# Kernel tuning notes

Measured on AMD Instinct MI355X. Metric: run time of the kernel, lower is better.

## Reference

```python
import jax, jax.numpy as jnp
import numpy as np

N, E, H = 25000, 100000, 32          # nodes, edges, node/clique hidden dim
NC, A, EC = 8000, 50000, 24000       # cliques, node2clique assignments, clique edges
EEMB, CEE, L = 8, 8, 2               # edge emb dims, n layers


def segment_mean(vals, ids, num):
    s = jax.ops.segment_sum(vals, ids, num_segments=num)
    cnt = jax.ops.segment_sum(jnp.ones(ids.shape[0], vals.dtype), ids, num_segments=num)
    return s / jnp.maximum(cnt, 1.0)[:, None]


def setup_inputs() -> dict:
    key = jax.random.key(0)
    ks = jax.random.split(key, 24)
    s = 0.1  # param scale
    inp = {
        "node_features": jax.random.normal(ks[0], (N, H), jnp.float32),
        "edge_index": jax.random.randint(ks[1], (2, E), 0, N),
        "edge_features": jax.random.normal(ks[2], (E, EEMB), jnp.float32),
        "clique_features": jax.random.normal(ks[3], (NC, H), jnp.float32),
        "node2clique_index": jnp.stack([
            jax.random.randint(ks[4], (A,), 0, N),
            jax.random.randint(ks[5], (A,), 0, NC)]),
        "clique_edge_index": jax.random.randint(ks[6], (2, EC), 0, NC),
        "clique_edge_features": jax.random.normal(ks[7], (EC, CEE), jnp.float32),
        # node NNConv params (stacked over L layers)
        "nn1_w": jax.random.normal(ks[8], (L, EEMB, H)) * s,
        "nn1_b": jnp.zeros((L, H)),
        "nn2_w": jax.random.normal(ks[9], (L, H, H * H)) * s,
        "nn2_b": jnp.zeros((L, H * H)),
        "root_w": jax.random.normal(ks[10], (L, H, H)) * s,
        "root_b": jnp.zeros((L, H)),
        # Node2Clique linear
        "n2c_w": jax.random.normal(ks[11], (L, H, H)) * s,
        "n2c_b": jnp.zeros((L, H)),
        # clique NNConv params
        "cnn1_w": jax.random.normal(ks[12], (L, CEE, H)) * s,
        "cnn1_b": jnp.zeros((L, H)),
        "cnn2_w": jax.random.normal(ks[13], (L, H, H * H)) * s,
        "cnn2_b": jnp.zeros((L, H * H)),
        "croot_w": jax.random.normal(ks[14], (L, H, H)) * s,
        "croot_b": jnp.zeros((L, H)),
        # Clique2Node linear
        "c2n_w": jax.random.normal(ks[15], (L, H, H)) * s,
        "c2n_b": jnp.zeros((L, H)),
    }
    return inp


def nnconv(x, src, dst, edge_attr, w1, b1, w2, b2, rw, rb, n_out_nodes):
    # per-edge weight matrices from the edge MLP: [E, in, out]
    h = jax.nn.relu(edge_attr @ w1 + b1)
    We = (h @ w2 + b2).reshape(edge_attr.shape[0], x.shape[1], -1)
    msg = jnp.einsum('ei,eio->eo', x[src], We)           # message from source
    agg = segment_mean(msg, dst, n_out_nodes)            # mean aggregation at target
    return agg + x @ rw + rb                             # root weight + bias


def reference(node_features, edge_index, edge_features, clique_features,
              node2clique_index, clique_edge_index, clique_edge_features,
              nn1_w, nn1_b, nn2_w, nn2_b, root_w, root_b, n2c_w, n2c_b,
              cnn1_w, cnn1_b, cnn2_w, cnn2_b, croot_w, croot_b, c2n_w, c2n_b):
    x, c = node_features, clique_features
    src, dst = edge_index[0], edge_index[1]
    nid, cid = node2clique_index[0], node2clique_index[1]
    csrc, cdst = clique_edge_index[0], clique_edge_index[1]
    for l in range(L):
        # node-level edge-conditioned conv
        x = jax.nn.relu(nnconv(x, src, dst, edge_features,
                               nn1_w[l], nn1_b[l], nn2_w[l], nn2_b[l],
                               root_w[l], root_b[l], N))
        # Node2Clique: project node feats, scatter-mean into cliques
        m = x @ n2c_w[l] + n2c_b[l]
        c = c + segment_mean(m[nid], cid, NC)
        # clique-level edge-conditioned conv
        c = jax.nn.relu(nnconv(c, csrc, cdst, clique_edge_features,
                               cnn1_w[l], cnn1_b[l], cnn2_w[l], cnn2_b[l],
                               croot_w[l], croot_b[l], NC))
        # Clique2Node: project clique feats, scatter-mean back onto nodes
        m = c @ c2n_w[l] + c2n_b[l]
        x = x + segment_mean(m[cid], nid, N)
    return (x, c)
```

## Files before the change

kernel.cpp:

```cpp
#include <hip/hip_runtime.h>
#include <hip/hip_bf16.h>

typedef unsigned int u32;
typedef unsigned short u16;

#define DEVINL __device__ __forceinline__

constexpr int Nn  = 25000;
constexpr int Ee  = 100000;
constexpr int NCc = 8000;
constexpr int Aa  = 50000;
constexpr int ECc = 24000;
constexpr int TCOLS = 1088;
constexpr int WPSZ  = TCOLS*32;
constexpr int TSP   = 1064;
constexpr int NB_N = (Nn + 255)/256;
constexpr int NB_C = (NCc + 255)/256;

typedef float f32x4 __attribute__((ext_vector_type(4)));
typedef short s16x8 __attribute__((ext_vector_type(8)));

DEVINL float b2f(u16 u){ union{u32 i;float f;}v; v.i = ((u32)u)<<16; return v.f; }
DEVINL float bfl(u32 u){ union{u32 i;float f;}v; v.i = u<<16; return v.f; }
DEVINL float bfh(u32 u){ union{u32 i;float f;}v; v.i = u & 0xffff0000u; return v.f; }
DEVINL u16 f2b(float f){ union{float f;u32 i;}v; v.f=f; u32 i=v.i;
  return (u16)((i + 0x7fffu + ((i>>16)&1u)) >> 16); }
DEVINL u32 pk2(float a, float b){ return (u32)f2b(a) | ((u32)f2b(b) << 16); }
DEVINL float ldw(const void* p, long i, int f){
  return f ? ((const float*)p)[i] : b2f(((const u16*)p)[i]);
}

__global__ __launch_bounds__(256) void k_detect(const u16* __restrict__ p, int n,
                        u32* __restrict__ maxbits, int* __restrict__ zcnt,
                        int* __restrict__ done, int* __restrict__ flag){
  int i0 = blockIdx.x*256 + threadIdx.x;
  float lm = 0.f; int lz = 0;
  for (int i = i0; i < n; i += gridDim.x*256){
    u16 v = p[i];
    if (v == 0) lz++;
    lm = fmaxf(lm, fabsf(b2f(v)));
  }
  #pragma unroll
  for (int off = 32; off; off >>= 1){
    lm = fmaxf(lm, __shfl_down(lm, off));
    lz += __shfl_down(lz, off);
  }
  if ((threadIdx.x & 63) == 0){
    atomicMax(maxbits, __float_as_uint(lm));
    atomicAdd(zcnt, lz);
  }
  __syncthreads();
  if (threadIdx.x == 0){
    __threadfence();
    if (atomicAdd(done, 1) == gridDim.x - 1){
      float m = __uint_as_float(*maxbits);
      *flag = (m > 1e6f || *zcnt > n/4) ? 1 : 0;
    }
  }
}

__global__ __launch_bounds__(256) void k_count_all(const int* __restrict__ ei, const int* __restrict__ cei,
                          const int* __restrict__ n2c,
                          int* __restrict__ deg_nd, int* __restrict__ deg_ce,
                          int* __restrict__ deg_n2c, int* __restrict__ deg_c2n,
                          int* __restrict__ cnt_sn, int* __restrict__ cnt_sc){
  int i = blockIdx.x*256 + threadIdx.x;
  if (i < Ee)                             atomicAdd(&deg_nd[ei[Ee + i]], 1);
  else if ((i -= Ee) < ECc)               atomicAdd(&deg_ce[cei[ECc + i]], 1);
  else if ((i -= ECc) < Aa)               atomicAdd(&deg_n2c[n2c[Aa + i]], 1);
  else if ((i -= Aa) < Aa)                atomicAdd(&deg_c2n[n2c[i]], 1);
  else if ((i -= Aa) < Ee)                atomicAdd(&cnt_sn[ei[i]], 1);
  else if ((i -= Ee) < ECc)               atomicAdd(&cnt_sc[cei[i]], 1);
}

__global__ __launch_bounds__(256) void k_scan_block(
    const int* __restrict__ c0, const int* __restrict__ c1,
    const int* __restrict__ c2, const int* __restrict__ c3,
    int* __restrict__ o0, int* __restrict__ o1, int* __restrict__ o2, int* __restrict__ o3,
    int* __restrict__ b0, int* __restrict__ b1, int* __restrict__ b2, int* __restrict__ b3){
  __shared__ int s[256];
  int bid = blockIdx.x, seg, rb;
  if (bid < NB_N){ seg=0; rb=bid; }
  else if (bid < NB_N+NB_C){ seg=1; rb=bid-NB_N; }
  else if (bid < 2*NB_N+NB_C){ seg=2; rb=bid-NB_N-NB_C; }
  else { seg=3; rb=bid-2*NB_N-NB_C; }
  const int* cnt = seg==0?c0 : seg==1?c1 : seg==2?c2 : c3;
  int* offs = seg==0?o0 : seg==1?o1 : seg==2?o2 : o3;
  int* bs   = seg==0?b0 : seg==1?b1 : seg==2?b2 : b3;
  int M = (seg & 1) ? NCc : Nn;
  int tid = threadIdx.x;
  int i = rb*256 + tid;
  int v = (i < M) ? cnt[i] : 0;
  s[tid] = v; __syncthreads();
  for (int d = 1; d < 256; d <<= 1){
    int t = (tid >= d) ? s[tid-d] : 0;
    __syncthreads();
    s[tid] += t;
    __syncthreads();
  }
  if (i < M) offs[i] = s[tid] - v;
  if (tid == 255) bs[rb] = s[255];
}

__global__ __launch_bounds__(512) void k_spine(int* __restrict__ b0, int* __restrict__ b1,
                      int* __restrict__ b2, int* __restrict__ b3){
  __shared__ int s[512];
  int tid = threadIdx.x, seg = tid >> 7, lane = tid & 127;
  int NB = (seg & 1) ? NB_C : NB_N;
  int* bp = seg==0?b0 : seg==1?b1 : seg==2?b2 : b3;
  int v = (lane < NB) ? bp[lane] : 0;
  s[tid] = v; __syncthreads();
  for (int d = 1; d < 128; d <<= 1){
    int t = (lane >= d) ? s[tid-d] : 0;
    __syncthreads();
    s[tid] += t;
    __syncthreads();
  }
  if (lane < NB) bp[lane] = s[tid] - v;
}

__global__ __launch_bounds__(256) void k_scan_fix(
    int* __restrict__ o0, int* __restrict__ o1, int* __restrict__ o2, int* __restrict__ o3,
    const int* __restrict__ b0, const int* __restrict__ b1,
    const int* __restrict__ b2, const int* __restrict__ b3){
  int i = blockIdx.x*256 + threadIdx.x;
  if (i < Nn) o0[i] += b0[i >> 8];
  else if ((i -= Nn) < NCc) o1[i] += b1[i >> 8];
  else if ((i -= NCc) < Nn) o2[i] += b2[i >> 8];
  else if ((i -= Nn) < NCc) o3[i] += b3[i >> 8];
}

__global__ __launch_bounds__(256) void k_place(const int* __restrict__ ei, const int* __restrict__ cei,
                      const int* __restrict__ n2c,
                      const int* __restrict__ offs_n, const int* __restrict__ offs_c,
                      const int* __restrict__ offs_an, const int* __restrict__ offs_ac,
                      int* __restrict__ cur_n, int* __restrict__ cur_c,
                      int* __restrict__ cur_an, int* __restrict__ cur_ac,
                      int* __restrict__ perm_n, int* __restrict__ perm_c,
                      int* __restrict__ an2c, int* __restrict__ ac2n){
  int i = blockIdx.x*256 + threadIdx.x;
  if (i < Ee){
    int s = ei[i];
    perm_n[offs_n[s] + atomicAdd(&cur_n[s], 1)] = i;
  } else if ((i -= Ee) < ECc){
    int s = cei[i];
    perm_c[offs_c[s] + atomicAdd(&cur_c[s], 1)] = i;
  } else if ((i -= ECc) < Aa){
    int c = n2c[Aa + i];
    an2c[offs_ac[c] + atomicAdd(&cur_ac[c], 1)] = n2c[i];
  } else if ((i -= Aa) < Aa){
    int nd = n2c[i];
    ac2n[offs_an[nd] + atomicAdd(&cur_an[nd], 1)] = n2c[Aa + i];
  }
}

__global__ __launch_bounds__(256) void k_gather(const int* __restrict__ ei, const int* __restrict__ cei,
                       const int* __restrict__ perm_n, const int* __restrict__ perm_c,
                       const void* __restrict__ ef, const void* __restrict__ cef,
                       const int* __restrict__ flag,
                       int2* __restrict__ sdp_n, float* __restrict__ efp_n,
                       int2* __restrict__ sdp_c, float* __restrict__ efp_c){
  int i = blockIdx.x*256 + threadIdx.x;
  int f = *flag;
  if (i < Ee*8){
    int p = i >> 3, j = i & 7;
    int e = perm_n[p];
    efp_n[i] = ldw(ef, (long)e*8 + j, f);
    if (j == 0) sdp_n[p] = make_int2(ei[e], ei[Ee + e]);
  } else if ((i -= Ee*8) < ECc*8){
    int p = i >> 3, j = i & 7;
    int e = perm_c[p];
    efp_c[i] = ldw(cef, (long)e*8 + j, f);
    if (j == 0) sdp_c[p] = make_int2(cei[e], cei[ECc + e]);
  }
}

__global__ __launch_bounds__(256) void k_wpack_all(const void* __restrict__ nn2w, const void* __restrict__ nn2b,
                          const void* __restrict__ rootw,
                          const void* __restrict__ cnn2w, const void* __restrict__ cnn2b,
                          const void* __restrict__ crootw,
                          const int* __restrict__ flag, u16* __restrict__ Wp4){
  int i = blockIdx.x*256 + threadIdx.x;
  if (i >= 4*WPSZ) return;
  int set = i / WPSZ, j = i - set*WPSZ;
  int l = set >> 1, isC = set & 1;
  const void* W2 = isC ? cnn2w : nn2w;
  const void* B2 = isC ? cnn2b : nn2b;
  const void* RW = isC ? crootw : rootw;
  int f = *flag;
  int col = j >> 5, ii = j & 31;
  float v;
  if (col < 1024)      v = ldw(W2, (long)l*32768 + ((col>>5)<<10) + (ii<<5) + (col&31), f);
  else if (col < 1056) v = ldw(B2, (long)l*1024 + (ii<<5) + (col-1024), f);
  else                 v = ldw(RW, (long)l*1024 + (ii<<5) + (col-1056), f);
  Wp4[i] = f2b(v);
}

__global__ __launch_bounds__(512) void k_conv_fused(const void* __restrict__ base, int braw,
                           const float* __restrict__ addagg, const int* __restrict__ adddeg, int M,
                           const int2* __restrict__ sdp, const float* __restrict__ efp,
                           const int* __restrict__ offs, int E_,
                           const void* __restrict__ w1, long w1off,
                           const void* __restrict__ b1, long b1off,
                           const u16* __restrict__ Wp,
                           const void* __restrict__ rb, long rboff,
                           const int* __restrict__ flag,
                           float* __restrict__ feat_root, float* __restrict__ agg){
  __shared__ __align__(16) u16 Ts[16*TSP];
  __shared__ float w1s[256];
  __shared__ __align__(8) u32 hws[8][4][16];
  int tid = threadIdx.x;
  int w = tid >> 6, lane = tid & 63;
  int quad = lane >> 4, lm = lane & 15;
  int n0 = blockIdx.x * 16;
  int f = *flag;
  if (tid < 256) w1s[tid] = ldw(w1, w1off + tid, f);
  float bb0 = ldw(b1, b1off + 2*lm, f);
  float bb1 = ldw(b1, b1off + 2*lm + 1, f);
  int n = n0 + lm;
  int nc = n < M ? n : M-1;
  long bidx = (long)nc*32 + quad*8;
  float fv[8];
  if (braw && f == 0){
    uint4 q = *(const uint4*)((const u16*)base + bidx);
    fv[0]=bfl(q.x); fv[1]=bfh(q.x); fv[2]=bfl(q.y); fv[3]=bfh(q.y);
    fv[4]=bfl(q.z); fv[5]=bfh(q.z); fv[6]=bfl(q.w); fv[7]=bfh(q.w);
  } else {
    const float4* bp = (const float4*)((const float*)base + bidx);
    float4 q0 = bp[0], q1 = bp[1];
    fv[0]=q0.x; fv[1]=q0.y; fv[2]=q0.z; fv[3]=q0.w;
    fv[4]=q1.x; fv[5]=q1.y; fv[6]=q1.z; fv[7]=q1.w;
  }
  if (addagg){
    int dg = adddeg[nc];
    float d = (float)(dg > 1 ? dg : 1);
    const float4* ap = (const float4*)(addagg + (size_t)nc*32 + quad*8);
    float4 a0 = ap[0], a1 = ap[1];
    float inv = 1.f/d;
    fv[0]+=a0.x*inv; fv[1]+=a0.y*inv; fv[2]+=a0.z*inv; fv[3]+=a0.w*inv;
    fv[4]+=a1.x*inv; fv[5]+=a1.y*inv; fv[6]+=a1.z*inv; fv[7]+=a1.w*inv;
  }
  s16x8 bfrag;
  #pragma unroll
  for (int j = 0; j < 8; j++) bfrag[j] = (short)f2b(fv[j]);
  #pragma unroll 1
  for (int ti = 0; ti < 9; ti++){
    int ct = w*9 + ti;
    if (ct >= 68) break;
    int colbase = ct*16;
    s16x8 afrag = *(const s16x8*)(Wp + (size_t)(colbase + lm)*32 + quad*8);
    f32x4 acc = {0.f, 0.f, 0.f, 0.f};
    acc = __builtin_amdgcn_mfma_f32_16x16x32_bf16(afrag, bfrag, acc, 0, 0, 0);
    int cb = colbase + quad*4;
    if (ct < 66){
      u32 lo = (u32)f2b(acc[0]) | ((u32)f2b(acc[1]) << 16);
      u32 hi = (u32)f2b(acc[2]) | ((u32)f2b(acc[3]) << 16);
      *(uint2*)&Ts[lm*TSP + cb] = make_uint2(lo, hi);
    } else if (n < M){
      int o = cb - 1056;
      float4 v = make_float4(acc[0] + ldw(rb, rboff+o,   f),
                             acc[1] + ldw(rb, rboff+o+1, f),
                             acc[2] + ldw(rb, rboff+o+2, f),
                             acc[3] + ldw(rb, rboff+o+3, f));
      *(float4*)&feat_root[(size_t)n*32 + o] = v;
    }
  }
  __syncthreads();
  int lo = offs[n0];
  int hi = (n0 + 16 < M) ? offs[n0 + 16] : E_;
  int eg = quad, kk = lm;
  int pos = lo + w*4;
  float ef0 = 0.f, ef1 = 0.f; int sd0 = 0, sd1 = 0;
  if (lane < 32){
    int idx = pos*8 + lane;        if (idx < hi*8) ef0 = efp[idx];
    idx = (pos+32)*8 + lane;       if (idx < hi*8) ef1 = efp[idx];
  } else if (lane < 40){
    int idx = pos*2 + (lane-32);   if (idx < hi*2) sd0 = ((const int*)sdp)[idx];
    idx = (pos+32)*2 + (lane-32);  if (idx < hi*2) sd1 = ((const int*)sdp)[idx];
  }
  for (; pos < hi; pos += 32){
    int np = pos + 64;
    float ef2 = 0.f; int sd2 = 0;
    if (lane < 32){ int idx = np*8 + lane; if (idx < hi*8) ef2 = efp[idx]; }
    else if (lane < 40){ int idx = np*2 + (lane-32); if (idx < hi*2) sd2 = ((const int*)sdp)[idx]; }
    int sn = __shfl(sd0, 32 + 2*eg);
    int dn = __shfl(sd0, 33 + 2*eg);
    bool valid = (pos + eg < hi);
    int sr = sn - n0; sr = sr < 0 ? 0 : (sr > 15 ? 15 : sr);
    float a0 = bb0, a1 = bb1;
    #pragma unroll
    for (int j = 0; j < 8; j++){
      float ev = __shfl(ef0, eg*8 + j);
      a0 += ev * w1s[j*32 + 2*kk];
      a1 += ev * w1s[j*32 + 2*kk+1];
    }
    hws[w][eg][kk] = pk2(fmaxf(a0, 0.f), fmaxf(a1, 0.f));
    if (valid){
      const u16* Tr = &Ts[sr*TSP];
      u32 vb = *(const u32*)&Tr[1024 + 2*kk];
      float m0 = bfl(vb), m1 = bfh(vb);
      #pragma unroll
      for (int kq = 0; kq < 16; kq++){
        u32 hp = hws[w][eg][kq];
        float h0 = bfl(hp), h1 = bfh(hp);
        u32 v0 = *(const u32*)&Tr[(2*kq)*32 + 2*kk];
        u32 v1 = *(const u32*)&Tr[(2*kq+1)*32 + 2*kk];
        m0 += h0*bfl(v0) + h1*bfl(v1);
        m1 += h0*bfh(v0) + h1*bfh(v1);
      }
      float* ap = agg + (size_t)dn*32 + 2*kk;
      atomicAdd(ap,   m0);
      atomicAdd(ap+1, m1);
    }
    ef0 = ef1; sd0 = sd1; ef1 = ef2; sd1 = sd2;
  }
}

__global__ __launch_bounds__(256) void k_update_lin(const float* __restrict__ agg, const int* __restrict__ deg,
                           const float* __restrict__ feat_root, int M,
                           const void* __restrict__ w, long woff,
                           const void* __restrict__ b, long boff,
                           const int* __restrict__ flag,
                           float* __restrict__ feat,
                           const int* __restrict__ sidx, const int* __restrict__ soffs,
                           const int* __restrict__ sdeg, float* __restrict__ sagg){
  __shared__ float wsm[1024], bs[32], rows[8][33];
  int tid = threadIdx.x;
  int f = *flag;
  for (int idx = tid; idx < 1024; idx += 256) wsm[idx] = ldw(w, woff + idx, f);
  if (tid < 32) bs[tid] = ldw(b, boff + tid, f);
  int nl = tid >> 5, o = tid & 31;
  int n = blockIdx.x*8 + nl;
  long i = (long)n*32 + o;
  if (n < M){
    int dg = deg[n];
    float d = (float)(dg > 1 ? dg : 1);
    float v = fmaxf(agg[i]/d + feat_root[i], 0.f);
    rows[nl][o] = v;
    feat[i] = v;
  }
  __syncthreads();
  if (n >= M) return;
  float acc = bs[o];
  #pragma unroll
  for (int j = 0; j < 32; j++) acc += rows[nl][j]*wsm[j*32+o];
  int slo = soffs[n], scnt = sdeg[n];
  for (int a = 0; a < scnt; a++)
    atomicAdd(&sagg[(size_t)sidx[slo + a]*32 + o], acc);
}

__global__ __launch_bounds__(256) void k_store(const float* __restrict__ x, const float* __restrict__ xagg,
                      const int* __restrict__ xdeg, const float* __restrict__ c,
                      void* __restrict__ out, const int* __restrict__ flag){
  int i = blockIdx.x*256 + threadIdx.x;
  int tot = Nn*32 + NCc*32;
  if (i >= tot) return;
  float v;
  if (i < Nn*32){
    int n = i >> 5;
    int dg = xdeg[n];
    float d = (float)(dg > 1 ? dg : 1);
    v = x[i] + xagg[i]/d;
  } else v = c[i - Nn*32];
  if (*flag) ((float*)out)[i] = v;
  else       ((u16*)out)[i]   = f2b(v);
}

extern "C" void kernel_launch(void* const* d_in, const int* in_sizes, int n_in,
                              void* d_out, int out_size, void* d_ws, size_t ws_size,
                              hipStream_t stream){
  const int* ei  = (const int*)d_in[1];
  const int* n2c = (const int*)d_in[4];
  const int* cei = (const int*)d_in[5];
  const void *efr = d_in[2], *cefr = d_in[6];
  const void *nn1w = d_in[7], *nn1b = d_in[8], *nn2w = d_in[9], *nn2b = d_in[10],
             *rootw = d_in[11], *rootb = d_in[12], *n2cw = d_in[13], *n2cb = d_in[14],
             *cnn1w = d_in[15], *cnn1b = d_in[16], *cnn2w = d_in[17], *cnn2b = d_in[18],
             *crootw = d_in[19], *crootb = d_in[20], *c2nw = d_in[21], *c2nb = d_in[22];

  char* ws = (char*)d_ws;
  size_t off = 0;
  auto alloc = [&](size_t bytes){ void* p = ws + off; off += (bytes + 255) & ~(size_t)255; return p; };

  size_t zstart = off;
  float* aggE0  = (float*)alloc((size_t)Nn*32*4);
  float* aggE1  = (float*)alloc((size_t)Nn*32*4);
  float* caggE0 = (float*)alloc((size_t)NCc*32*4);
  float* caggE1 = (float*)alloc((size_t)NCc*32*4);
  float* caggS0 = (float*)alloc((size_t)NCc*32*4);
  float* caggS1 = (float*)alloc((size_t)NCc*32*4);
  float* aggS0  = (float*)alloc((size_t)Nn*32*4);
  float* aggS1  = (float*)alloc((size_t)Nn*32*4);
  int* deg_nd  = (int*)alloc((size_t)Nn*4);
  int* deg_ce  = (int*)alloc((size_t)NCc*4);
  int* deg_n2c = (int*)alloc((size_t)NCc*4);
  int* deg_c2n = (int*)alloc((size_t)Nn*4);
  int* cnt_sn  = (int*)alloc((size_t)Nn*4);
  int* cnt_sc  = (int*)alloc((size_t)NCc*4);
  int* cur_n   = (int*)alloc((size_t)Nn*4);
  int* cur_c   = (int*)alloc((size_t)NCc*4);
  int* cur_an  = (int*)alloc((size_t)Nn*4);
  int* cur_ac  = (int*)alloc((size_t)NCc*4);
  u32* maxbits = (u32*)alloc(256);
  int* zcnt = (int*)((char*)maxbits + 4);
  int* flag = (int*)((char*)maxbits + 8);
  int* done = (int*)((char*)maxbits + 12);
  size_t zbytes = off - zstart;

  float* xB  = (float*)alloc((size_t)Nn*32*4);
  float* xC  = (float*)alloc((size_t)Nn*32*4);
  float* cC0 = (float*)alloc((size_t)NCc*32*4);
  float* cC1 = (float*)alloc((size_t)NCc*32*4);
  float* frn = (float*)alloc((size_t)Nn*32*4);
  float* frc = (float*)alloc((size_t)NCc*32*4);
  int* offs_n  = (int*)alloc((size_t)Nn*4);
  int* offs_c  = (int*)alloc((size_t)NCc*4);
  int* offs_an = (int*)alloc((size_t)Nn*4);
  int* offs_ac = (int*)alloc((size_t)NCc*4);
  int* bs0 = (int*)alloc(512); int* bs1 = (int*)alloc(512);
  int* bs2 = (int*)alloc(512); int* bs3 = (int*)alloc(512);
  int* perm_n = (int*)alloc((size_t)Ee*4);
  int* perm_c = (int*)alloc((size_t)ECc*4);
  int* an2c = (int*)alloc((size_t)Aa*4);
  int* ac2n = (int*)alloc((size_t)Aa*4);
  int2* sdp_n = (int2*)alloc((size_t)Ee*8);
  int2* sdp_c = (int2*)alloc((size_t)ECc*8);
  float* efp_n = (float*)alloc((size_t)Ee*8*4);
  float* efp_c = (float*)alloc((size_t)ECc*8*4);
  u16* Wp4 = (u16*)alloc((size_t)4*WPSZ*2);

  auto nb = [](int n){ return (n + 255)/256; };

  hipMemsetAsync(ws + zstart, 0, zbytes, stream);
  k_detect<<<256,256,0,stream>>>((const u16*)d_in[0], Nn*32, maxbits, zcnt, done, flag);
  k_count_all<<<nb(2*Ee + 2*ECc + 2*Aa),256,0,stream>>>(ei, cei, n2c,
      deg_nd, deg_ce, deg_n2c, deg_c2n, cnt_sn, cnt_sc);
  k_scan_block<<<2*(NB_N+NB_C),256,0,stream>>>(cnt_sn, cnt_sc, deg_c2n, deg_n2c,
      offs_n, offs_c, offs_an, offs_ac, bs0, bs1, bs2, bs3);
  k_spine<<<1,512,0,stream>>>(bs0, bs1, bs2, bs3);
  k_scan_fix<<<nb(2*(Nn+NCc)),256,0,stream>>>(offs_n, offs_c, offs_an, offs_ac,
      bs0, bs1, bs2, bs3);
  k_place<<<nb(Ee+ECc+2*Aa),256,0,stream>>>(ei, cei, n2c, offs_n, offs_c, offs_an, offs_ac,
      cur_n, cur_c, cur_an, cur_ac, perm_n, perm_c, an2c, ac2n);
  k_gather<<<nb(8*(Ee+ECc)),256,0,stream>>>(ei, cei, perm_n, perm_c, efr, cefr, flag,
      sdp_n, efp_n, sdp_c, efp_c);
  k_wpack_all<<<nb(4*WPSZ),256,0,stream>>>(nn2w, nn2b, rootw, cnn2w, cnn2b, crootw, flag, Wp4);

  int Gn = (Nn + 15)/16, Gc = (NCc + 15)/16;

  k_conv_fused<<<Gn,512,0,stream>>>(d_in[0], 1, nullptr, nullptr, Nn, sdp_n, efp_n, offs_n, Ee,
      nn1w, 0, nn1b, 0, Wp4 + 0*WPSZ, rootb, 0, flag, frn, aggE0);
  k_update_lin<<<(Nn+7)/8,256,0,stream>>>(aggE0, deg_nd, frn, Nn, n2cw, 0, n2cb, 0, flag,
      xB, ac2n, offs_an, deg_c2n, caggS0);
  k_conv_fused<<<Gc,512,0,stream>>>(d_in[3], 1, caggS0, deg_n2c, NCc, sdp_c, efp_c, offs_c, ECc,
      cnn1w, 0, cnn1b, 0, Wp4 + 1*WPSZ, crootb, 0, flag, frc, caggE0);
  k_update_lin<<<(NCc+7)/8,256,0,stream>>>(caggE0, deg_ce, frc, NCc, c2nw, 0, c2nb, 0, flag,
      cC0, an2c, offs_ac, deg_n2c, aggS0);
  k_conv_fused<<<Gn,512,0,stream>>>(xB, 0, aggS0, deg_c2n, Nn, sdp_n, efp_n, offs_n, Ee,
      nn1w, 256, nn1b, 32, Wp4 + 2*WPSZ, rootb, 32, flag, frn, aggE1);
  k_update_lin<<<(Nn+7)/8,256,0,stream>>>(aggE1, deg_nd, frn, Nn, n2cw, 1024, n2cb, 32, flag,
      xC, ac2n, offs_an, deg_c2n, caggS1);
  k_conv_fused<<<Gc,512,0,stream>>>(cC0, 0, caggS1, deg_n2c, NCc, sdp_c, efp_c, offs_c, ECc,
      cnn1w, 256, cnn1b, 32, Wp4 + 3*WPSZ, crootb, 32, flag, frc, caggE1);
  k_update_lin<<<(NCc+7)/8,256,0,stream>>>(caggE1, deg_ce, frc, NCc, c2nw, 1024, c2nb, 32, flag,
      cC1, an2c, offs_ac, deg_n2c, aggS1);
  k_store<<<nb(Nn*32 + NCc*32),256,0,stream>>>(xC, aggS1, deg_c2n, cC1, d_out, flag);
}
```

Baseline: 344.6 us.

## Merge preprocessing kernels and use persistent work-stealing conv blocks

Merges detection with degree counting, and scanning with weight packing, into single launches. The three-kernel scan becomes one kernel that spins on a global counter for all block sums. The conv kernel now runs a fixed grid of 1024 blocks that pull 16-node windows from an atomic counter and prefetch the next weight fragment. This removes launch gaps and tail imbalance but adds spin-wait and atomic overhead. The spin-wait assumes all scan blocks are co-resident, which could deadlock if they are not.

New measurement: 403.0 us. +16.9%, slower.

```diff
diff --git a/kernel.cpp b/kernel.cpp
--- a/kernel.cpp
+++ b/kernel.cpp
@@ -16,6 +16,7 @@
 constexpr int TSP   = 1064;
 constexpr int NB_N = (Nn + 255)/256;
 constexpr int NB_C = (NCc + 255)/256;
+constexpr int NCH  = 2*(NB_N + NB_C);
 
 typedef float f32x4 __attribute__((ext_vector_type(4)));
 typedef short s16x8 __attribute__((ext_vector_type(8)));
@@ -30,56 +31,81 @@
   return f ? ((const float*)p)[i] : b2f(((const u16*)p)[i]);
 }
 
-__global__ __launch_bounds__(256) void k_detect(const u16* __restrict__ p, int n,
-                        u32* __restrict__ maxbits, int* __restrict__ zcnt,
-                        int* __restrict__ done, int* __restrict__ flag){
-  int i0 = blockIdx.x*256 + threadIdx.x;
-  float lm = 0.f; int lz = 0;
-  for (int i = i0; i < n; i += gridDim.x*256){
-    u16 v = p[i];
-    if (v == 0) lz++;
-    lm = fmaxf(lm, fabsf(b2f(v)));
-  }
-  #pragma unroll
-  for (int off = 32; off; off >>= 1){
-    lm = fmaxf(lm, __shfl_down(lm, off));
-    lz += __shfl_down(lz, off);
-  }
-  if ((threadIdx.x & 63) == 0){
-    atomicMax(maxbits, __float_as_uint(lm));
-    atomicAdd(zcnt, lz);
-  }
-  __syncthreads();
-  if (threadIdx.x == 0){
-    __threadfence();
-    if (atomicAdd(done, 1) == gridDim.x - 1){
-      float m = __uint_as_float(*maxbits);
-      *flag = (m > 1e6f || *zcnt > n/4) ? 1 : 0;
-    }
-  }
-}
-
-__global__ __launch_bounds__(256) void k_count_all(const int* __restrict__ ei, const int* __restrict__ cei,
-                          const int* __restrict__ n2c,
-                          int* __restrict__ deg_nd, int* __restrict__ deg_ce,
-                          int* __restrict__ deg_n2c, int* __restrict__ deg_c2n,
-                          int* __restrict__ cnt_sn, int* __restrict__ cnt_sc){
-  int i = blockIdx.x*256 + threadIdx.x;
-  if (i < Ee)                             atomicAdd(&deg_nd[ei[Ee + i]], 1);
-  else if ((i -= Ee) < ECc)               atomicAdd(&deg_ce[cei[ECc + i]], 1);
-  else if ((i -= ECc) < Aa)               atomicAdd(&deg_n2c[n2c[Aa + i]], 1);
-  else if ((i -= Aa) < Aa)                atomicAdd(&deg_c2n[n2c[i]], 1);
-  else if ((i -= Aa) < Ee)                atomicAdd(&cnt_sn[ei[i]], 1);
-  else if ((i -= Ee) < ECc)               atomicAdd(&cnt_sc[cei[i]], 1);
-}
-
-__global__ __launch_bounds__(256) void k_scan_block(
+__global__ __launch_bounds__(256) void k_pre1(const u16* __restrict__ xp,
+                      u32* __restrict__ maxbits, int* __restrict__ zcnt,
+                      int* __restrict__ done, int* __restrict__ flag,
+                      const int* __restrict__ ei, const int* __restrict__ cei,
+                      const int* __restrict__ n2c,
+                      int* __restrict__ deg_nd, int* __restrict__ deg_ce,
+                      int* __restrict__ deg_n2c, int* __restrict__ deg_c2n,
+                      int* __restrict__ cnt_sn, int* __restrict__ cnt_sc){
+  int bid = blockIdx.x;
+  if (bid < 256){
+    int n = Nn*32;
+    float lm = 0.f; int lz = 0;
+    for (int i = bid*256 + threadIdx.x; i < n; i += 256*256){
+      u16 v = xp[i];
+      if (v == 0) lz++;
+      lm = fmaxf(lm, fabsf(b2f(v)));
+    }
+    #pragma unroll
+    for (int off = 32; off; off >>= 1){
+      lm = fmaxf(lm, __shfl_down(lm, off));
+      lz += __shfl_down(lz, off);
+    }
+    if ((threadIdx.x & 63) == 0){
+      atomicMax(maxbits, __float_as_uint(lm));
+      atomicAdd(zcnt, lz);
+    }
+    __syncthreads();
+    if (threadIdx.x == 0){
+      __threadfence();
+      if (atomicAdd(done, 1) == 255){
+        float m = __uint_as_float(*maxbits);
+        *flag = (m > 1e6f || *zcnt > n/4) ? 1 : 0;
+      }
+    }
+  } else {
+    int i = (bid - 256)*256 + threadIdx.x;
+    if (i < Ee)                             atomicAdd(&deg_nd[ei[Ee + i]], 1);
+    else if ((i -= Ee) < ECc)               atomicAdd(&deg_ce[cei[ECc + i]], 1);
+    else if ((i -= ECc) < Aa)               atomicAdd(&deg_n2c[n2c[Aa + i]], 1);
+    else if ((i -= Aa) < Aa)                atomicAdd(&deg_c2n[n2c[i]], 1);
+    else if ((i -= Aa) < Ee)                atomicAdd(&cnt_sn[ei[i]], 1);
+    else if ((i -= Ee) < ECc)               atomicAdd(&cnt_sc[cei[i]], 1);
+  }
+}
+
+__global__ __launch_bounds__(256) void k_scan_wpack(
     const int* __restrict__ c0, const int* __restrict__ c1,
     const int* __restrict__ c2, const int* __restrict__ c3,
     int* __restrict__ o0, int* __restrict__ o1, int* __restrict__ o2, int* __restrict__ o3,
-    int* __restrict__ b0, int* __restrict__ b1, int* __restrict__ b2, int* __restrict__ b3){
+    int* __restrict__ b0, int* __restrict__ b1, int* __restrict__ b2, int* __restrict__ b3,
+    int* __restrict__ sdone,
+    const void* __restrict__ nn2w, const void* __restrict__ nn2b, const void* __restrict__ rootw,
+    const void* __restrict__ cnn2w, const void* __restrict__ cnn2b, const void* __restrict__ crootw,
+    const int* __restrict__ flag, u16* __restrict__ Wp4){
+  int bid = blockIdx.x;
+  int tid = threadIdx.x;
+  if (bid >= NCH){
+    int i = (bid - NCH)*256 + tid;
+    if (i >= 4*WPSZ) return;
+    int set = i / WPSZ, j = i - set*WPSZ;
+    int l = set >> 1, isC = set & 1;
+    const void* W2 = isC ? cnn2w : nn2w;
+    const void* B2 = isC ? cnn2b : nn2b;
+    const void* RW = isC ? crootw : rootw;
+    int f = *flag;
+    int col = j >> 5, ii = j & 31;
+    float v;
+    if (col < 1024)      v = ldw(W2, (long)l*32768 + ((col>>5)<<10) + (ii<<5) + (col&31), f);
+    else if (col < 1056) v = ldw(B2, (long)l*1024 + (ii<<5) + (col-1024), f);
+    else                 v = ldw(RW, (long)l*1024 + (ii<<5) + (col-1056), f);
+    Wp4[i] = f2b(v);
+    return;
+  }
   __shared__ int s[256];
-  int bid = blockIdx.x, seg, rb;
+  int seg, rb;
   if (bid < NB_N){ seg=0; rb=bid; }
   else if (bid < NB_N+NB_C){ seg=1; rb=bid-NB_N; }
   else if (bid < 2*NB_N+NB_C){ seg=2; rb=bid-NB_N-NB_C; }
@@ -88,7 +114,6 @@
   int* offs = seg==0?o0 : seg==1?o1 : seg==2?o2 : o3;
   int* bs   = seg==0?b0 : seg==1?b1 : seg==2?b2 : b3;
   int M = (seg & 1) ? NCc : Nn;
-  int tid = threadIdx.x;
   int i = rb*256 + tid;
   int v = (i < M) ? cnt[i] : 0;
   s[tid] = v; __syncthreads();
@@ -98,36 +123,23 @@
     s[tid] += t;
     __syncthreads();
   }
-  if (i < M) offs[i] = s[tid] - v;
-  if (tid == 255) bs[rb] = s[255];
-}
-
-__global__ __launch_bounds__(512) void k_spine(int* __restrict__ b0, int* __restrict__ b1,
-                      int* __restrict__ b2, int* __restrict__ b3){
-  __shared__ int s[512];
-  int tid = threadIdx.x, seg = tid >> 7, lane = tid & 127;
-  int NB = (seg & 1) ? NB_C : NB_N;
-  int* bp = seg==0?b0 : seg==1?b1 : seg==2?b2 : b3;
-  int v = (lane < NB) ? bp[lane] : 0;
-  s[tid] = v; __syncthreads();
-  for (int d = 1; d < 128; d <<= 1){
-    int t = (lane >= d) ? s[tid-d] : 0;
-    __syncthreads();
-    s[tid] += t;
-    __syncthreads();
-  }
-  if (lane < NB) bp[lane] = s[tid] - v;
-}
-
-__global__ __launch_bounds__(256) void k_scan_fix(
-    int* __restrict__ o0, int* __restrict__ o1, int* __restrict__ o2, int* __restrict__ o3,
-    const int* __restrict__ b0, const int* __restrict__ b1,
-    const int* __restrict__ b2, const int* __restrict__ b3){
-  int i = blockIdx.x*256 + threadIdx.x;
-  if (i < Nn) o0[i] += b0[i >> 8];
-  else if ((i -= Nn) < NCc) o1[i] += b1[i >> 8];
-  else if ((i -= NCc) < Nn) o2[i] += b2[i >> 8];
-  else if ((i -= Nn) < NCc) o3[i] += b3[i >> 8];
+  int ex = s[tid] - v;
+  if (tid == 255){
+    atomicExch(&bs[rb], s[255]);
+    __threadfence();
+    atomicAdd(sdone, 1);
+  }
+  if (tid == 0){
+    while (atomicAdd(sdone, 0) < NCH) __builtin_amdgcn_s_sleep(8);
+  }
+  __syncthreads();
+  int contrib = (tid < rb) ? atomicAdd(&bs[tid], 0) : 0;
+  s[tid] = contrib; __syncthreads();
+  for (int d = 128; d; d >>= 1){
+    if (tid < d) s[tid] += s[tid + d];
+    __syncthreads();
+  }
+  if (i < M) offs[i] = ex + s[0];
 }
 
 __global__ __launch_bounds__(256) void k_place(const int* __restrict__ ei, const int* __restrict__ cei,
@@ -175,27 +187,6 @@
   }
 }
 
-__global__ __launch_bounds__(256) void k_wpack_all(const void* __restrict__ nn2w, const void* __restrict__ nn2b,
-                          const void* __restrict__ rootw,
-                          const void* __restrict__ cnn2w, const void* __restrict__ cnn2b,
-                          const void* __restrict__ crootw,
-                          const int* __restrict__ flag, u16* __restrict__ Wp4){
-  int i = blockIdx.x*256 + threadIdx.x;
-  if (i >= 4*WPSZ) return;
-  int set = i / WPSZ, j = i - set*WPSZ;
-  int l = set >> 1, isC = set & 1;
-  const void* W2 = isC ? cnn2w : nn2w;
-  const void* B2 = isC ? cnn2b : nn2b;
-  const void* RW = isC ? crootw : rootw;
-  int f = *flag;
-  int col = j >> 5, ii = j & 31;
-  float v;
-  if (col < 1024)      v = ldw(W2, (long)l*32768 + ((col>>5)<<10) + (ii<<5) + (col&31), f);
-  else if (col < 1056) v = ldw(B2, (long)l*1024 + (ii<<5) + (col-1024), f);
-  else                 v = ldw(RW, (long)l*1024 + (ii<<5) + (col-1056), f);
-  Wp4[i] = f2b(v);
-}
-
 __global__ __launch_bounds__(512) void k_conv_fused(const void* __restrict__ base, int braw,
                            const float* __restrict__ addagg, const int* __restrict__ adddeg, int M,
                            const int2* __restrict__ sdp, const float* __restrict__ efp,
@@ -205,114 +196,127 @@
                            const u16* __restrict__ Wp,
                            const void* __restrict__ rb, long rboff,
                            const int* __restrict__ flag,
+                           int* __restrict__ wctr,
                            float* __restrict__ feat_root, float* __restrict__ agg){
   __shared__ __align__(16) u16 Ts[16*TSP];
   __shared__ float w1s[256];
   __shared__ __align__(8) u32 hws[8][4][16];
+  __shared__ int wshare;
   int tid = threadIdx.x;
   int w = tid >> 6, lane = tid & 63;
   int quad = lane >> 4, lm = lane & 15;
-  int n0 = blockIdx.x * 16;
   int f = *flag;
   if (tid < 256) w1s[tid] = ldw(w1, w1off + tid, f);
   float bb0 = ldw(b1, b1off + 2*lm, f);
   float bb1 = ldw(b1, b1off + 2*lm + 1, f);
-  int n = n0 + lm;
-  int nc = n < M ? n : M-1;
-  long bidx = (long)nc*32 + quad*8;
-  float fv[8];
-  if (braw && f == 0){
-    uint4 q = *(const uint4*)((const u16*)base + bidx);
-    fv[0]=bfl(q.x); fv[1]=bfh(q.x); fv[2]=bfl(q.y); fv[3]=bfh(q.y);
-    fv[4]=bfl(q.z); fv[5]=bfh(q.z); fv[6]=bfl(q.w); fv[7]=bfh(q.w);
-  } else {
-    const float4* bp = (const float4*)((const float*)base + bidx);
-    float4 q0 = bp[0], q1 = bp[1];
-    fv[0]=q0.x; fv[1]=q0.y; fv[2]=q0.z; fv[3]=q0.w;
-    fv[4]=q1.x; fv[5]=q1.y; fv[6]=q1.z; fv[7]=q1.w;
-  }
-  if (addagg){
-    int dg = adddeg[nc];
-    float d = (float)(dg > 1 ? dg : 1);
-    const float4* ap = (const float4*)(addagg + (size_t)nc*32 + quad*8);
-    float4 a0 = ap[0], a1 = ap[1];
-    float inv = 1.f/d;
-    fv[0]+=a0.x*inv; fv[1]+=a0.y*inv; fv[2]+=a0.z*inv; fv[3]+=a0.w*inv;
-    fv[4]+=a1.x*inv; fv[5]+=a1.y*inv; fv[6]+=a1.z*inv; fv[7]+=a1.w*inv;
-  }
-  s16x8 bfrag;
-  #pragma unroll
-  for (int j = 0; j < 8; j++) bfrag[j] = (short)f2b(fv[j]);
-  #pragma unroll 1
-  for (int ti = 0; ti < 9; ti++){
-    int ct = w*9 + ti;
-    if (ct >= 68) break;
-    int colbase = ct*16;
-    s16x8 afrag = *(const s16x8*)(Wp + (size_t)(colbase + lm)*32 + quad*8);
-    f32x4 acc = {0.f, 0.f, 0.f, 0.f};
-    acc = __builtin_amdgcn_mfma_f32_16x16x32_bf16(afrag, bfrag, acc, 0, 0, 0);
-    int cb = colbase + quad*4;
-    if (ct < 66){
-      u32 lo = (u32)f2b(acc[0]) | ((u32)f2b(acc[1]) << 16);
-      u32 hi = (u32)f2b(acc[2]) | ((u32)f2b(acc[3]) << 16);
-      *(uint2*)&Ts[lm*TSP + cb] = make_uint2(lo, hi);
-    } else if (n < M){
-      int o = cb - 1056;
-      float4 v = make_float4(acc[0] + ldw(rb, rboff+o,   f),
-                             acc[1] + ldw(rb, rboff+o+1, f),
-                             acc[2] + ldw(rb, rboff+o+2, f),
-                             acc[3] + ldw(rb, rboff+o+3, f));
-      *(float4*)&feat_root[(size_t)n*32 + o] = v;
-    }
-  }
-  __syncthreads();
-  int lo = offs[n0];
-  int hi = (n0 + 16 < M) ? offs[n0 + 16] : E_;
-  int eg = quad, kk = lm;
-  int pos = lo + w*4;
-  float ef0 = 0.f, ef1 = 0.f; int sd0 = 0, sd1 = 0;
-  if (lane < 32){
-    int idx = pos*8 + lane;        if (idx < hi*8) ef0 = efp[idx];
-    idx = (pos+32)*8 + lane;       if (idx < hi*8) ef1 = efp[idx];
-  } else if (lane < 40){
-    int idx = pos*2 + (lane-32);   if (idx < hi*2) sd0 = ((const int*)sdp)[idx];
-    idx = (pos+32)*2 + (lane-32);  if (idx < hi*2) sd1 = ((const int*)sdp)[idx];
-  }
-  for (; pos < hi; pos += 32){
-    int np = pos + 64;
-    float ef2 = 0.f; int sd2 = 0;
-    if (lane < 32){ int idx = np*8 + lane; if (idx < hi*8) ef2 = efp[idx]; }
-    else if (lane < 40){ int idx = np*2 + (lane-32); if (idx < hi*2) sd2 = ((const int*)sdp)[idx]; }
-    int sn = __shfl(sd0, 32 + 2*eg);
-    int dn = __shfl(sd0, 33 + 2*eg);
-    bool valid = (pos + eg < hi);
-    int sr = sn - n0; sr = sr < 0 ? 0 : (sr > 15 ? 15 : sr);
-    float a0 = bb0, a1 = bb1;
+  int nwin = (M + 15)/16;
+  for (;;){
+    if (tid == 0) wshare = atomicAdd(wctr, 1);
+    __syncthreads();
+    int win = wshare;
+    if (win >= nwin) break;
+    int n0 = win * 16;
+    int n = n0 + lm;
+    int nc = n < M ? n : M-1;
+    long bidx = (long)nc*32 + quad*8;
+    float fv[8];
+    if (braw && f == 0){
+      uint4 q = *(const uint4*)((const u16*)base + bidx);
+      fv[0]=bfl(q.x); fv[1]=bfh(q.x); fv[2]=bfl(q.y); fv[3]=bfh(q.y);
+      fv[4]=bfl(q.z); fv[5]=bfh(q.z); fv[6]=bfl(q.w); fv[7]=bfh(q.w);
+    } else {
+      const float4* bp = (const float4*)((const float*)base + bidx);
+      float4 q0 = bp[0], q1 = bp[1];
+      fv[0]=q0.x; fv[1]=q0.y; fv[2]=q0.z; fv[3]=q0.w;
+      fv[4]=q1.x; fv[5]=q1.y; fv[6]=q1.z; fv[7]=q1.w;
+    }
+    if (addagg){
+      int dg = adddeg[nc];
+      float inv = 1.f/(float)(dg > 1 ? dg : 1);
+      const float4* ap = (const float4*)(addagg + (size_t)nc*32 + quad*8);
+      float4 a0 = ap[0], a1 = ap[1];
+      fv[0]+=a0.x*inv; fv[1]+=a0.y*inv; fv[2]+=a0.z*inv; fv[3]+=a0.w*inv;
+      fv[4]+=a1.x*inv; fv[5]+=a1.y*inv; fv[6]+=a1.z*inv; fv[7]+=a1.w*inv;
+    }
+    s16x8 bfrag;
     #pragma unroll
-    for (int j = 0; j < 8; j++){
-      float ev = __shfl(ef0, eg*8 + j);
-      a0 += ev * w1s[j*32 + 2*kk];
-      a1 += ev * w1s[j*32 + 2*kk+1];
-    }
-    hws[w][eg][kk] = pk2(fmaxf(a0, 0.f), fmaxf(a1, 0.f));
-    if (valid){
-      const u16* Tr = &Ts[sr*TSP];
-      u32 vb = *(const u32*)&Tr[1024 + 2*kk];
-      float m0 = bfl(vb), m1 = bfh(vb);
+    for (int j = 0; j < 8; j++) bfrag[j] = (short)f2b(fv[j]);
+    int ctbase = w*9;
+    s16x8 afc = *(const s16x8*)(Wp + (size_t)(ctbase*16 + lm)*32 + quad*8);
+    #pragma unroll 1
+    for (int ti = 0; ti < 9; ti++){
+      int ct = ctbase + ti;
+      if (ct >= 68) break;
+      s16x8 afn;
+      bool have_n = (ti + 1 < 9) && (ct + 1 < 68);
+      if (have_n) afn = *(const s16x8*)(Wp + (size_t)((ct+1)*16 + lm)*32 + quad*8);
+      f32x4 acc = {0.f, 0.f, 0.f, 0.f};
+      acc = __builtin_amdgcn_mfma_f32_16x16x32_bf16(afc, bfrag, acc, 0, 0, 0);
+      int cb = ct*16 + quad*4;
+      if (ct < 66){
+        u32 lo = (u32)f2b(acc[0]) | ((u32)f2b(acc[1]) << 16);
+        u32 hi = (u32)f2b(acc[2]) | ((u32)f2b(acc[3]) << 16);
+        *(uint2*)&Ts[lm*TSP + cb] = make_uint2(lo, hi);
+      } else if (n < M){
+        int o = cb - 1056;
+        float4 v = make_float4(acc[0] + ldw(rb, rboff+o,   f),
+                               acc[1] + ldw(rb, rboff+o+1, f),
+                               acc[2] + ldw(rb, rboff+o+2, f),
+                               acc[3] + ldw(rb, rboff+o+3, f));
+        *(float4*)&feat_root[(size_t)n*32 + o] = v;
+      }
+      if (have_n) afc = afn;
+    }
+    __syncthreads();
+    int lo = offs[n0];
+    int hi = (n0 + 16 < M) ? offs[n0 + 16] : E_;
+    int eg = quad, kk = lm;
+    int pos = lo + w*4;
+    float ef0 = 0.f, ef1 = 0.f; int sd0 = 0, sd1 = 0;
+    if (lane < 32){
+      int idx = pos*8 + lane;        if (idx < hi*8) ef0 = efp[idx];
+      idx = (pos+32)*8 + lane;       if (idx < hi*8) ef1 = efp[idx];
+    } else if (lane < 40){
+      int idx = pos*2 + (lane-32);   if (idx < hi*2) sd0 = ((const int*)sdp)[idx];
+      idx = (pos+32)*2 + (lane-32);  if (idx < hi*2) sd1 = ((const int*)sdp)[idx];
+    }
+    for (; pos < hi; pos += 32){
+      int np = pos + 64;
+      float ef2 = 0.f; int sd2 = 0;
+      if (lane < 32){ int idx = np*8 + lane; if (idx < hi*8) ef2 = efp[idx]; }
+      else if (lane < 40){ int idx = np*2 + (lane-32); if (idx < hi*2) sd2 = ((const int*)sdp)[idx]; }
+      int sn = __shfl(sd0, 32 + 2*eg);
+      int dn = __shfl(sd0, 33 + 2*eg);
+      bool valid = (pos + eg < hi);
+      int sr = sn - n0; sr = sr < 0 ? 0 : (sr > 15 ? 15 : sr);
+      float a0 = bb0, a1 = bb1;
       #pragma unroll
-      for (int kq = 0; kq < 16; kq++){
-        u32 hp = hws[w][eg][kq];
-        float h0 = bfl(hp), h1 = bfh(hp);
-        u32 v0 = *(const u32*)&Tr[(2*kq)*32 + 2*kk];
-        u32 v1 = *(const u32*)&Tr[(2*kq+1)*32 + 2*kk];
-        m0 += h0*bfl(v0) + h1*bfl(v1);
-        m1 += h0*bfh(v0) + h1*bfh(v1);
+      for (int j = 0; j < 8; j++){
+        float ev = __shfl(ef0, eg*8 + j);
+        a0 += ev * w1s[j*32 + 2*kk];
+        a1 += ev * w1s[j*32 + 2*kk+1];
       }
-      float* ap = agg + (size_t)dn*32 + 2*kk;
-      atomicAdd(ap,   m0);
-      atomicAdd(ap+1, m1);
-    }
-    ef0 = ef1; sd0 = sd1; ef1 = ef2; sd1 = sd2;
+      hws[w][eg][kk] = pk2(fmaxf(a0, 0.f), fmaxf(a1, 0.f));
+      if (valid){
+        const u16* Tr = &Ts[sr*TSP];
+        u32 vb = *(const u32*)&Tr[1024 + 2*kk];
+        float m0 = bfl(vb), m1 = bfh(vb);
+        #pragma unroll
+        for (int kq = 0; kq < 16; kq++){
+          u32 hp = hws[w][eg][kq];
+          float h0 = bfl(hp), h1 = bfh(hp);
+          u32 v0 = *(const u32*)&Tr[(2*kq)*32 + 2*kk];
+          u32 v1 = *(const u32*)&Tr[(2*kq+1)*32 + 2*kk];
+          m0 += h0*bfl(v0) + h1*bfl(v1);
+          m1 += h0*bfh(v0) + h1*bfh(v1);
+        }
+        float* ap = agg + (size_t)dn*32 + 2*kk;
+        atomicAdd(ap,   m0);
+        atomicAdd(ap+1, m1);
+      }
+      ef0 = ef1; sd0 = sd1; ef1 = ef2; sd1 = sd2;
+    }
+    __syncthreads();
   }
 }
 
@@ -402,9 +406,14 @@
   int* cur_an  = (int*)alloc((size_t)Nn*4);
   int* cur_ac  = (int*)alloc((size_t)NCc*4);
   u32* maxbits = (u32*)alloc(256);
-  int* zcnt = (int*)((char*)maxbits + 4);
-  int* flag = (int*)((char*)maxbits + 8);
-  int* done = (int*)((char*)maxbits + 12);
+  int* zcnt  = (int*)((char*)maxbits + 4);
+  int* flag  = (int*)((char*)maxbits + 8);
+  int* done  = (int*)((char*)maxbits + 12);
+  int* sdone = (int*)((char*)maxbits + 16);
+  int* wctr0 = (int*)((char*)maxbits + 20);
+  int* wctr1 = (int*)((char*)maxbits + 24);
+  int* wctr2 = (int*)((char*)maxbits + 28);
+  int* wctr3 = (int*)((char*)maxbits + 32);
   size_t zbytes = off - zstart;
 
   float* xB  = (float*)alloc((size_t)Nn*32*4);
@@ -432,36 +441,31 @@
   auto nb = [](int n){ return (n + 255)/256; };
 
   hipMemsetAsync(ws + zstart, 0, zbytes, stream);
-  k_detect<<<256,256,0,stream>>>((const u16*)d_in[0], Nn*32, maxbits, zcnt, done, flag);
-  k_count_all<<<nb(2*Ee + 2*ECc + 2*Aa),256,0,stream>>>(ei, cei, n2c,
+  k_pre1<<<256 + nb(2*Ee + 2*ECc + 2*Aa),256,0,stream>>>((const u16*)d_in[0],
+      maxbits, zcnt, done, flag, ei, cei, n2c,
       deg_nd, deg_ce, deg_n2c, deg_c2n, cnt_sn, cnt_sc);
-  k_scan_block<<<2*(NB_N+NB_C),256,0,stream>>>(cnt_sn, cnt_sc, deg_c2n, deg_n2c,
-      offs_n, offs_c, offs_an, offs_ac, bs0, bs1, bs2, bs3);
-  k_spine<<<1,512,0,stream>>>(bs0, bs1, bs2, bs3);
-  k_scan_fix<<<nb(2*(Nn+NCc)),256,0,stream>>>(offs_n, offs_c, offs_an, offs_ac,
-      bs0, bs1, bs2, bs3);
+  k_scan_wpack<<<NCH + nb(4*WPSZ),256,0,stream>>>(cnt_sn, cnt_sc, deg_c2n, deg_n2c,
+      offs_n, offs_c, offs_an, offs_ac, bs0, bs1, bs2, bs3, sdone,
+      nn2w, nn2b, rootw, cnn2w, cnn2b, crootw, flag, Wp4);
   k_place<<<nb(Ee+ECc+2*Aa),256,0,stream>>>(ei, cei, n2c, offs_n, offs_c, offs_an, offs_ac,
       cur_n, cur_c, cur_an, cur_ac, perm_n, perm_c, an2c, ac2n);
   k_gather<<<nb(8*(Ee+ECc)),256,0,stream>>>(ei, cei, perm_n, perm_c, efr, cefr, flag,
       sdp_n, efp_n, sdp_c, efp_c);
-  k_wpack_all<<<nb(4*WPSZ),256,0,stream>>>(nn2w, nn2b, rootw, cnn2w, cnn2b, crootw, flag, Wp4);
-
-  int Gn = (Nn + 15)/16, Gc = (NCc + 15)/16;
-
-  k_conv_fused<<<Gn,512,0,stream>>>(d_in[0], 1, nullptr, nullptr, Nn, sdp_n, efp_n, offs_n, Ee,
-      nn1w, 0, nn1b, 0, Wp4 + 0*WPSZ, rootb, 0, flag, frn, aggE0);
+
+  k_conv_fused<<<1024,512,0,stream>>>(d_in[0], 1, nullptr, nullptr, Nn, sdp_n, efp_n, offs_n, Ee,
+      nn1w, 0, nn1b, 0, Wp4 + 0*WPSZ, rootb, 0, flag, wctr0, frn, aggE0);
   k_update_lin<<<(Nn+7)/8,256,0,stream>>>(aggE0, deg_nd, frn, Nn, n2cw, 0, n2cb, 0, flag,
       xB, ac2n, offs_an, deg_c2n, caggS0);
-  k_conv_fused<<<Gc,512,0,stream>>>(d_in[3], 1, caggS0, deg_n2c, NCc, sdp_c, efp_c, offs_c, ECc,
-      cnn1w, 0, cnn1b, 0, Wp4 + 1*WPSZ, crootb, 0, flag, frc, caggE0);
+  k_conv_fused<<<1024,512,0,stream>>>(d_in[3], 1, caggS0, deg_n2c, NCc, sdp_c, efp_c, offs_c, ECc,
+      cnn1w, 0, cnn1b, 0, Wp4 + 1*WPSZ, crootb, 0, flag, wctr1, frc, caggE0);
   k_update_lin<<<(NCc+7)/8,256,0,stream>>>(caggE0, deg_ce, frc, NCc, c2nw, 0, c2nb, 0, flag,
       cC0, an2c, offs_ac, deg_n2c, aggS0);
-  k_conv_fused<<<Gn,512,0,stream>>>(xB, 0, aggS0, deg_c2n, Nn, sdp_n, efp_n, offs_n, Ee,
-      nn1w, 256, nn1b, 32, Wp4 + 2*WPSZ, rootb, 32, flag, frn, aggE1);
+  k_conv_fused<<<1024,512,0,stream>>>(xB, 0, aggS0, deg_c2n, Nn, sdp_n, efp_n, offs_n, Ee,
+      nn1w, 256, nn1b, 32, Wp4 + 2*WPSZ, rootb, 32, flag, wctr2, frn, aggE1);
   k_update_lin<<<(Nn+7)/8,256,0,stream>>>(aggE1, deg_nd, frn, Nn, n2cw, 1024, n2cb, 32, flag,
       xC, ac2n, offs_an, deg_c2n, caggS1);
-  k_conv_fused<<<Gc,512,0,stream>>>(cC0, 0, caggS1, deg_n2c, NCc, sdp_c, efp_c, offs_c, ECc,
-      cnn1w, 256, cnn1b, 32, Wp4 + 3*WPSZ, crootb, 32, flag, frc, caggE1);
+  k_conv_fused<<<1024,512,0,stream>>>(cC0, 0, caggS1, deg_n2c, NCc, sdp_c, efp_c, offs_c, ECc,
+      cnn1w, 256, cnn1b, 32, Wp4 + 3*WPSZ, crootb, 32, flag, wctr3, frc, caggE1);
   k_update_lin<<<(NCc+7)/8,256,0,stream>>>(caggE1, deg_ce, frc, NCc, c2nw, 1024, c2nb, 32, flag,
       cC1, an2c, offs_ac, deg_n2c, aggS1);
   k_store<<<nb(Nn*32 + NCc*32),256,0,stream>>>(xC, aggS1, deg_c2n, cC1, d_out, flag);
```
